# Performance work log

Hardware: AMD Instinct MI355X
Metric: run time of the kernel (lower is better)

Reference implementation:

```python
import jax, jax.numpy as jnp
import numpy as np

ENC_DIM, DEC_DIM, ATT_DIM = 2048, 512, 512
B, L = 64, 1024


def setup_inputs() -> dict:
    key = jax.random.key(0)
    ks = jax.random.split(key, 8)
    s_enc = 1.0 / np.sqrt(ENC_DIM)
    s_dec = 1.0 / np.sqrt(DEC_DIM)
    s_att = 1.0 / np.sqrt(ATT_DIM)
    return {
        "encoder_out": jax.random.normal(ks[0], (B, L, ENC_DIM), jnp.float32),
        "decoder_hidden": jax.random.normal(ks[1], (B, DEC_DIM), jnp.float32),
        "W_enc": jax.random.uniform(ks[2], (ENC_DIM, ATT_DIM), jnp.float32, -s_enc, s_enc),
        "b_enc": jax.random.uniform(ks[3], (ATT_DIM,), jnp.float32, -s_enc, s_enc),
        "W_dec": jax.random.uniform(ks[4], (DEC_DIM, ATT_DIM), jnp.float32, -s_dec, s_dec),
        "b_dec": jax.random.uniform(ks[5], (ATT_DIM,), jnp.float32, -s_dec, s_dec),
        "W_full": jax.random.uniform(ks[6], (ATT_DIM,), jnp.float32, -s_att, s_att),
        "b_full": jax.random.uniform(ks[7], (), jnp.float32, -s_att, s_att),
    }


def reference(encoder_out, decoder_hidden, W_enc, b_enc, W_dec, b_dec, W_full, b_full):
    # att1: [B, L, A]
    att1 = jnp.einsum('ble,ea->bla', encoder_out, W_enc) + b_enc
    # att2: [B, A]
    att2 = decoder_hidden @ W_dec + b_dec
    # scores: [B, L]
    att = jnp.einsum('bla,a->bl', jnp.tanh(att1 + att2[:, None, :]), W_full) + b_full
    alpha = jax.nn.softmax(att, axis=1)
    # NOTE: faithful to source -- weighted sum is over att1, not encoder_out.
    attention_weighted_encoding = jnp.einsum('bla,bl->ba', att1, alpha)
    return attention_weighted_encoding, alpha
```

## Files before the change

kernel.cpp:

```cpp
#include <hip/hip_runtime.h>
#include <hip/hip_bf16.h>


#define Bn 64
#define Ln 1024
#define En 2048
#define An 512
#define TM 64
#define NTILES (Ln/TM)
#define AWE_OFF 0
#define ALPHA_OFF (Bn*An)
#define TILEB 8192

using short8 = __attribute__((ext_vector_type(8))) short;
using f32x4  = __attribute__((ext_vector_type(4))) float;

__device__ inline short f2bf(float x){
    unsigned u = __builtin_bit_cast(unsigned, x);
    unsigned r = (u + 0x7fffu + ((u >> 16) & 1u)) >> 16;
    return (short)r;
}
__device__ inline float tanh_fast(float x){
    return 2.0f * __frcp_rn(1.0f + __expf(-2.0f * x)) - 1.0f;
}

__global__ __launch_bounds__(256) void k_prep(const float* __restrict__ W,
                                              unsigned short* __restrict__ Wp,
                                              const float* __restrict__ dh,
                                              const float* __restrict__ Wd,
                                              const float* __restrict__ bd,
                                              float* __restrict__ att2){
    __shared__ float dl[512];
    int blk = blockIdx.x, tid = threadIdx.x;
    if (blk < 512){
        int t = blk * 256 + tid;
        int f = t >> 6, lane = t & 63;
        int kb = f >> 5, nc = f & 31;
        int k0 = kb * 32 + (lane >> 4) * 8;
        int col = nc * 16 + (lane & 15);
        short8 v;
#pragma unroll
        for (int j = 0; j < 8; ++j)
            v[j] = f2bf(W[(size_t)(k0 + j) * An + col]);
        *(short8*)(Wp + (size_t)f * 512 + lane * 8) = v;
    } else {
        int b = blk - 512;
        dl[tid]       = dh[b * 512 + tid];
        dl[tid + 256] = dh[b * 512 + tid + 256];
        __syncthreads();
        for (int a = tid; a < An; a += 256){
            float s = bd[a];
            for (int k = 0; k < 512; ++k)
                s = fmaf(dl[k], Wd[(size_t)k * An + a], s);
            att2[b * An + a] = s;
        }
    }
}


#define MFMA(a, b, c) __builtin_amdgcn_mfma_f32_16x16x32_bf16((a), (b), (c), 0, 0, 0)

#define BLOAD(P)                                                              \
    { int pc = (P) > 31 ? 31 : (P);                                           \
      const unsigned short* bp = Bbase + (size_t)pc * 32768;                  \
      f00 = *(const short8*)(bp);                                             \
      f01 = *(const short8*)(bp + 512);                                       \
      f02 = *(const short8*)(bp + 1024);                                      \
      f03 = *(const short8*)(bp + 1536);                                      \
      f10 = *(const short8*)(bp + 16384);                                     \
      f11 = *(const short8*)(bp + 16384 + 512);                               \
      f12 = *(const short8*)(bp + 16384 + 1024);                              \
      f13 = *(const short8*)(bp + 16384 + 1536); }

#define STAGE(Q, R0, R1)                                                      \
    { short8 sv;                                                              \
      sv[0] = f2bf(R0.x); sv[1] = f2bf(R0.y);                                 \
      sv[2] = f2bf(R0.z); sv[3] = f2bf(R0.w);                                 \
      sv[4] = f2bf(R1.x); sv[5] = f2bf(R1.y);                                 \
      sv[6] = f2bf(R1.z); sv[7] = f2bf(R1.w);                                 \
      *(short8*)(swp + (Q) * TILEB) = sv; }

#define MFMAS(Q)                                                              \
    __builtin_amdgcn_s_setprio(1);                                            \
    _Pragma("unroll")                                                         \
    for (int mi = 0; mi < 4; ++mi){                                           \
        short8 af0 = *(const short8*)(as0 + (Q) * TILEB + mi * 2048);         \
        short8 af1 = *(const short8*)(as1 + (Q) * TILEB + mi * 2048);         \
        acc[mi][0] = MFMA(af0, f00, acc[mi][0]);                              \
        acc[mi][1] = MFMA(af0, f01, acc[mi][1]);                              \
        acc[mi][2] = MFMA(af0, f02, acc[mi][2]);                              \
        acc[mi][3] = MFMA(af0, f03, acc[mi][3]);                              \
        acc[mi][0] = MFMA(af1, f10, acc[mi][0]);                              \
        acc[mi][1] = MFMA(af1, f11, acc[mi][1]);                              \
        acc[mi][2] = MFMA(af1, f12, acc[mi][2]);                              \
        acc[mi][3] = MFMA(af1, f13, acc[mi][3]);                              \
    }                                                                         \
    __builtin_amdgcn_s_setprio(0);

#define PBAR                                                                  \
    __builtin_amdgcn_sched_barrier(0);                                        \
    asm volatile("s_waitcnt lgkmcnt(0)");                                     \
    __builtin_amdgcn_s_barrier();                                             \
    __builtin_amdgcn_sched_barrier(0)

__global__ __launch_bounds__(1024)
void k_main(const float* __restrict__ enc, const unsigned short* __restrict__ Wp,
            const float* __restrict__ benc, const float* __restrict__ att2,
            const float* __restrict__ wfull, float* __restrict__ out,
            float* __restrict__ pawe_ws, float* __restrict__ ms_ws){
    const int wg   = blockIdx.x;
    const int b    = wg >> 4;
    const int tile = wg & 15;
    const int l0   = tile * TM;
    const int tid  = threadIdx.x;
    const int lane = tid & 63, w = tid >> 6;
    const bool cons = (w < 8);

    __shared__ alignas(16) unsigned short Alds[4][TM * 64];
    __shared__ float red[8][TM];
    __shared__ float plds[TM];
    char* const alds = (char*)Alds;

    const int ptid  = tid & 511;
    const int srow  = ptid >> 3;
    const int sbyte = srow * 128 + (((ptid & 7) * 16) ^ ((srow & 7) << 4));
    char* const swp = alds + sbyte;
    const float* apt = enc + ((size_t)(b * Ln + l0 + srow)) * En + (ptid & 7) * 8;

    const unsigned short* Bbase = Wp + (size_t)((w & 7) * 4) * 512 + lane * 8;
    const int arow = lane & 15;
    const int akb  = (lane >> 4) * 16;
    const int sw   = (arow & 7) << 4;
    const char* const as0 = alds + arow * 128 + (akb ^ sw);
    const char* const as1 = alds + arow * 128 + ((64 + akb) ^ sw);

    f32x4 acc[4][4];
#pragma unroll
    for (int mi = 0; mi < 4; ++mi)
#pragma unroll
        for (int ni = 0; ni < 4; ++ni)
            acc[mi][ni] = (f32x4){0.f, 0.f, 0.f, 0.f};

    if (cons){
        short8 f00, f01, f02, f03, f10, f11, f12, f13;
        PBAR;
        for (int sp = 0; sp < 8; ++sp){
            const int p = sp * 4;
            BLOAD(p)        MFMAS(0)
            BLOAD(p + 1)    MFMAS(1)
            PBAR;
            BLOAD(p + 2)    MFMAS(2)
            BLOAD(p + 3)    MFMAS(3)
            PBAR;
        }
    } else {
        float4 ra0 = *(const float4*)(apt);
        float4 ra1 = *(const float4*)(apt + 4);
        float4 rb0 = *(const float4*)(apt + 64);
        float4 rb1 = *(const float4*)(apt + 68);
        STAGE(0, ra0, ra1)
        STAGE(1, rb0, rb1)
        ra0 = *(const float4*)(apt + 2 * 64);
        ra1 = *(const float4*)(apt + 2 * 64 + 4);
        rb0 = *(const float4*)(apt + 3 * 64);
        rb1 = *(const float4*)(apt + 3 * 64 + 4);
        PBAR;
        for (int sp = 0; sp < 8; ++sp){
            const int p = sp * 4;
            {
                STAGE(2, ra0, ra1)
                STAGE(3, rb0, rb1)
                int t0 = p + 4 > 31 ? 31 : p + 4;
                int t1 = p + 5 > 31 ? 31 : p + 5;
                ra0 = *(const float4*)(apt + t0 * 64);
                ra1 = *(const float4*)(apt + t0 * 64 + 4);
                rb0 = *(const float4*)(apt + t1 * 64);
                rb1 = *(const float4*)(apt + t1 * 64 + 4);
            }
            PBAR;
            {
                STAGE(0, ra0, ra1)
                STAGE(1, rb0, rb1)
                int t0 = p + 6 > 31 ? 31 : p + 6;
                int t1 = p + 7 > 31 ? 31 : p + 7;
                ra0 = *(const float4*)(apt + t0 * 64);
                ra1 = *(const float4*)(apt + t0 * 64 + 4);
                rb0 = *(const float4*)(apt + t1 * 64);
                rb1 = *(const float4*)(apt + t1 * 64 + 4);
            }
            PBAR;
        }
    }

    float tsum[4][4];
    if (cons){
        float be[4], a2[4], wfv[4];
        const int cbase = (w & 7) * 64 + (lane & 15);
#pragma unroll
        for (int ni = 0; ni < 4; ++ni){
            int c = cbase + ni * 16;
            be[ni]  = benc[c];
            a2[ni]  = att2[b * An + c];
            wfv[ni] = wfull[c];
        }
#pragma unroll
        for (int mi = 0; mi < 4; ++mi)
#pragma unroll
            for (int j = 0; j < 4; ++j)
                tsum[mi][j] = 0.f;
#pragma unroll
        for (int mi = 0; mi < 4; ++mi)
#pragma unroll
            for (int ni = 0; ni < 4; ++ni)
#pragma unroll
                for (int j = 0; j < 4; ++j){
                    float vv = acc[mi][ni][j] + be[ni];
                    acc[mi][ni][j] = vv;
                    tsum[mi][j] += tanh_fast(vv + a2[ni]) * wfv[ni];
                }
#pragma unroll
        for (int mi = 0; mi < 4; ++mi)
#pragma unroll
            for (int j = 0; j < 4; ++j){
                float t = tsum[mi][j];
                t += __shfl_xor(t, 1); t += __shfl_xor(t, 2);
                t += __shfl_xor(t, 4); t += __shfl_xor(t, 8);
                if ((lane & 15) == 0)
                    red[w][mi * 16 + (lane >> 4) * 4 + j] = t;
            }
    }
    __syncthreads();

    if (tid < 64){
        float s = 0.f;
#pragma unroll
        for (int k = 0; k < 8; ++k)
            s += red[k][tid];
        out[ALPHA_OFF + b * Ln + l0 + tid] = s;
        float m = s;
        m = fmaxf(m, __shfl_xor(m, 1));  m = fmaxf(m, __shfl_xor(m, 2));
        m = fmaxf(m, __shfl_xor(m, 4));  m = fmaxf(m, __shfl_xor(m, 8));
        m = fmaxf(m, __shfl_xor(m, 16)); m = fmaxf(m, __shfl_xor(m, 32));
        float pv = __expf(s - m);
        float sm = pv;
        sm += __shfl_xor(sm, 1);  sm += __shfl_xor(sm, 2);
        sm += __shfl_xor(sm, 4);  sm += __shfl_xor(sm, 8);
        sm += __shfl_xor(sm, 16); sm += __shfl_xor(sm, 32);
        plds[tid] = pv;
        if (tid == 0){ ms_ws[wg * 2] = m; ms_ws[wg * 2 + 1] = sm; }
    }
    __syncthreads();

    if (cons){
        float pp[4];
#pragma unroll
        for (int ni = 0; ni < 4; ++ni) pp[ni] = 0.f;
#pragma unroll
        for (int mi = 0; mi < 4; ++mi)
#pragma unroll
            for (int j = 0; j < 4; ++j){
                float pr = plds[mi * 16 + (lane >> 4) * 4 + j];
#pragma unroll
                for (int ni = 0; ni < 4; ++ni)
                    pp[ni] += pr * acc[mi][ni][j];
            }
#pragma unroll
        for (int ni = 0; ni < 4; ++ni){
            pp[ni] += __shfl_xor(pp[ni], 16);
            pp[ni] += __shfl_xor(pp[ni], 32);
        }
        if (lane < 16){
#pragma unroll
            for (int ni = 0; ni < 4; ++ni)
                pawe_ws[(size_t)wg * An + (w & 7) * 64 + ni * 16 + lane] = pp[ni];
        }
    }
}

__global__ __launch_bounds__(256) void k_final(const float* __restrict__ pawe,
                                               const float* __restrict__ ms,
                                               float* __restrict__ out){
    int b = blockIdx.x, tid = threadIdx.x;
    __shared__ float scale[NTILES];
    __shared__ float sh[2];
    if (tid < 64){
        int lane = tid;
        float m = -1e30f, su = 0.f;
        if (lane < NTILES){ m = ms[(b * NTILES + lane) * 2]; su = ms[(b * NTILES + lane) * 2 + 1]; }
        float mm = m;
        mm = fmaxf(mm, __shfl_xor(mm, 1)); mm = fmaxf(mm, __shfl_xor(mm, 2));
        mm = fmaxf(mm, __shfl_xor(mm, 4)); mm = fmaxf(mm, __shfl_xor(mm, 8));
        float sc = (lane < NTILES) ? su * __expf(m - mm) : 0.f;
        float tot = sc;
        tot += __shfl_xor(tot, 1); tot += __shfl_xor(tot, 2);
        tot += __shfl_xor(tot, 4); tot += __shfl_xor(tot, 8);
        if (lane < NTILES) scale[lane] = __expf(m - mm);
        if (lane == 0){ sh[0] = 1.0f / tot; sh[1] = mm; }
    }
    __syncthreads();
    float inv = sh[0], mm = sh[1];
    for (int a = tid; a < An; a += 256){
        float s = 0.f;
#pragma unroll
        for (int t = 0; t < NTILES; ++t)
            s += pawe[((size_t)(b * NTILES + t)) * An + a] * scale[t];
        out[AWE_OFF + b * An + a] = s * inv;
    }
    for (int l = tid; l < Ln; l += 256){
        float s = out[ALPHA_OFF + b * Ln + l];
        out[ALPHA_OFF + b * Ln + l] = __expf(s - mm) * inv;
    }
}

extern "C" void kernel_launch(void* const* d_in, const int* in_sizes, int n_in,
                              void* d_out, int out_size, void* d_ws, size_t ws_size,
                              hipStream_t stream){
    const float* enc   = (const float*)d_in[0];
    const float* dh    = (const float*)d_in[1];
    const float* Wenc  = (const float*)d_in[2];
    const float* benc  = (const float*)d_in[3];
    const float* Wdec  = (const float*)d_in[4];
    const float* bdec  = (const float*)d_in[5];
    const float* wfull = (const float*)d_in[6];
    float* out = (float*)d_out;

    char* ws = (char*)d_ws;
    unsigned short* Wp = (unsigned short*)ws;
    float* att2 = (float*)(ws + (2u << 20));
    float* pawe = (float*)(ws + (2u << 20) + (128u << 10));
    float* msb  = (float*)(ws + (4u << 20) + (128u << 10));

    k_prep<<<576, 256, 0, stream>>>(Wenc, Wp, dh, Wdec, bdec, att2);
    k_main<<<Bn * NTILES, 1024, 0, stream>>>(enc, Wp, benc, att2, wfull, out, pawe, msb);
    k_final<<<Bn, 256, 0, stream>>>(pawe, msb, out);
}
```

Baseline: 258.2 us.

## Merge producer and consumer waves so each wave stages A and runs MFMAs

The main kernel no longer splits its 16 waves into 8 loader waves (global fp32 load, bf16 convert, LDS store) and 8 MFMA waves. It now launches 512 threads per block, and every wave both stages the encoder tile into LDS and issues the weight loads and MFMAs, interleaved inside one loop. Launch bounds change to (512, 4) to allow several blocks per CU. This is meant to remove idle loader waves and rely on multiple resident blocks for latency hiding, at the cost of higher per-wave register pressure and less explicit producer/consumer overlap.

```diff
diff --git a/kernel.cpp b/kernel.cpp
--- a/kernel.cpp
+++ b/kernel.cpp
@@ -60,7 +60,7 @@
 
 #define MFMA(a, b, c) __builtin_amdgcn_mfma_f32_16x16x32_bf16((a), (b), (c), 0, 0, 0)
 
-#define BLOAD(P)                                                              \
+#define BLOADF(P)                                                             \
     { int pc = (P) > 31 ? 31 : (P);                                           \
       const unsigned short* bp = Bbase + (size_t)pc * 32768;                  \
       f00 = *(const short8*)(bp);                                             \
@@ -103,7 +103,7 @@
     __builtin_amdgcn_s_barrier();                                             \
     __builtin_amdgcn_sched_barrier(0)
 
-__global__ __launch_bounds__(1024)
+__global__ __launch_bounds__(512, 4)
 void k_main(const float* __restrict__ enc, const unsigned short* __restrict__ Wp,
             const float* __restrict__ benc, const float* __restrict__ att2,
             const float* __restrict__ wfull, float* __restrict__ out,
@@ -114,121 +114,119 @@
     const int l0   = tile * TM;
     const int tid  = threadIdx.x;
     const int lane = tid & 63, w = tid >> 6;
-    const bool cons = (w < 8);
 
     __shared__ alignas(16) unsigned short Alds[4][TM * 64];
     __shared__ float red[8][TM];
     __shared__ float plds[TM];
     char* const alds = (char*)Alds;
 
-    const int ptid  = tid & 511;
-    const int srow  = ptid >> 3;
-    const int sbyte = srow * 128 + (((ptid & 7) * 16) ^ ((srow & 7) << 4));
+    f32x4 acc[4][4];
+#pragma unroll
+    for (int mi = 0; mi < 4; ++mi)
+#pragma unroll
+        for (int ni = 0; ni < 4; ++ni)
+            acc[mi][ni] = (f32x4){0.f, 0.f, 0.f, 0.f};
+
+    const int srow  = tid >> 3;
+    const int sbyte = srow * 128 + (((tid & 7) * 16) ^ ((srow & 7) << 4));
     char* const swp = alds + sbyte;
-    const float* apt = enc + ((size_t)(b * Ln + l0 + srow)) * En + (ptid & 7) * 8;
-
-    const unsigned short* Bbase = Wp + (size_t)((w & 7) * 4) * 512 + lane * 8;
+    const float* apt = enc + ((size_t)(b * Ln + l0 + srow)) * En + (tid & 7) * 8;
+
+    const unsigned short* Bbase = Wp + (size_t)(w * 4) * 512 + lane * 8;
+
     const int arow = lane & 15;
     const int akb  = (lane >> 4) * 16;
     const int sw   = (arow & 7) << 4;
     const char* const as0 = alds + arow * 128 + (akb ^ sw);
     const char* const as1 = alds + arow * 128 + ((64 + akb) ^ sw);
 
-    f32x4 acc[4][4];
+    short8 f00, f01, f02, f03, f10, f11, f12, f13;
+
+    float4 ra0 = *(const float4*)(apt);
+    float4 ra1 = *(const float4*)(apt + 4);
+    float4 rb0 = *(const float4*)(apt + 64);
+    float4 rb1 = *(const float4*)(apt + 68);
+    STAGE(0, ra0, ra1)
+    STAGE(1, rb0, rb1)
+    ra0 = *(const float4*)(apt + 2 * 64);
+    ra1 = *(const float4*)(apt + 2 * 64 + 4);
+    rb0 = *(const float4*)(apt + 3 * 64);
+    rb1 = *(const float4*)(apt + 3 * 64 + 4);
+
+    for (int p = 0; p < 32; p += 4){
+        PBAR;
+        {
+            BLOADF(p)
+            STAGE(2, ra0, ra1)
+            STAGE(3, rb0, rb1)
+            int t0 = p + 4 > 31 ? 31 : p + 4;
+            int t1 = p + 5 > 31 ? 31 : p + 5;
+            ra0 = *(const float4*)(apt + t0 * 64);
+            ra1 = *(const float4*)(apt + t0 * 64 + 4);
+            rb0 = *(const float4*)(apt + t1 * 64);
+            rb1 = *(const float4*)(apt + t1 * 64 + 4);
+            MFMAS(0)
+        }
+        {
+            BLOADF(p + 1)
+            MFMAS(1)
+        }
+        PBAR;
+        {
+            BLOADF(p + 2)
+            STAGE(0, ra0, ra1)
+            STAGE(1, rb0, rb1)
+            int t0 = p + 6 > 31 ? 31 : p + 6;
+            int t1 = p + 7 > 31 ? 31 : p + 7;
+            ra0 = *(const float4*)(apt + t0 * 64);
+            ra1 = *(const float4*)(apt + t0 * 64 + 4);
+            rb0 = *(const float4*)(apt + t1 * 64);
+            rb1 = *(const float4*)(apt + t1 * 64 + 4);
+            MFMAS(2)
+        }
+        {
+            BLOADF(p + 3)
+            MFMAS(3)
+        }
+    }
+
+    float be[4], a2[4], wfv[4];
+    const int cbase = w * 64 + (lane & 15);
+#pragma unroll
+    for (int ni = 0; ni < 4; ++ni){
+        int c = cbase + ni * 16;
+        be[ni]  = benc[c];
+        a2[ni]  = att2[b * An + c];
+        wfv[ni] = wfull[c];
+    }
+
+    float tsum[4][4];
+#pragma unroll
+    for (int mi = 0; mi < 4; ++mi)
+#pragma unroll
+        for (int j = 0; j < 4; ++j)
+            tsum[mi][j] = 0.f;
 #pragma unroll
     for (int mi = 0; mi < 4; ++mi)
 #pragma unroll
         for (int ni = 0; ni < 4; ++ni)
-            acc[mi][ni] = (f32x4){0.f, 0.f, 0.f, 0.f};
-
-    if (cons){
-        short8 f00, f01, f02, f03, f10, f11, f12, f13;
-        PBAR;
-        for (int sp = 0; sp < 8; ++sp){
-            const int p = sp * 4;
-            BLOAD(p)        MFMAS(0)
-            BLOAD(p + 1)    MFMAS(1)
-            PBAR;
-            BLOAD(p + 2)    MFMAS(2)
-            BLOAD(p + 3)    MFMAS(3)
-            PBAR;
-        }
-    } else {
-        float4 ra0 = *(const float4*)(apt);
-        float4 ra1 = *(const float4*)(apt + 4);
-        float4 rb0 = *(const float4*)(apt + 64);
-        float4 rb1 = *(const float4*)(apt + 68);
-        STAGE(0, ra0, ra1)
-        STAGE(1, rb0, rb1)
-        ra0 = *(const float4*)(apt + 2 * 64);
-        ra1 = *(const float4*)(apt + 2 * 64 + 4);
-        rb0 = *(const float4*)(apt + 3 * 64);
-        rb1 = *(const float4*)(apt + 3 * 64 + 4);
-        PBAR;
-        for (int sp = 0; sp < 8; ++sp){
-            const int p = sp * 4;
-            {
-                STAGE(2, ra0, ra1)
-                STAGE(3, rb0, rb1)
-                int t0 = p + 4 > 31 ? 31 : p + 4;
-                int t1 = p + 5 > 31 ? 31 : p + 5;
-                ra0 = *(const float4*)(apt + t0 * 64);
-                ra1 = *(const float4*)(apt + t0 * 64 + 4);
-                rb0 = *(const float4*)(apt + t1 * 64);
-                rb1 = *(const float4*)(apt + t1 * 64 + 4);
+#pragma unroll
+            for (int j = 0; j < 4; ++j){
+                float vv = acc[mi][ni][j] + be[ni];
+                acc[mi][ni][j] = vv;
+                tsum[mi][j] += tanh_fast(vv + a2[ni]) * wfv[ni];
             }
-            PBAR;
-            {
-                STAGE(0, ra0, ra1)
-                STAGE(1, rb0, rb1)
-                int t0 = p + 6 > 31 ? 31 : p + 6;
-                int t1 = p + 7 > 31 ? 31 : p + 7;
-                ra0 = *(const float4*)(apt + t0 * 64);
-                ra1 = *(const float4*)(apt + t0 * 64 + 4);
-                rb0 = *(const float4*)(apt + t1 * 64);
-                rb1 = *(const float4*)(apt + t1 * 64 + 4);
-            }
-            PBAR;
-        }
-    }
-
-    float tsum[4][4];
-    if (cons){
-        float be[4], a2[4], wfv[4];
-        const int cbase = (w & 7) * 64 + (lane & 15);
-#pragma unroll
-        for (int ni = 0; ni < 4; ++ni){
-            int c = cbase + ni * 16;
-            be[ni]  = benc[c];
-            a2[ni]  = att2[b * An + c];
-            wfv[ni] = wfull[c];
-        }
-#pragma unroll
-        for (int mi = 0; mi < 4; ++mi)
-#pragma unroll
-            for (int j = 0; j < 4; ++j)
-                tsum[mi][j] = 0.f;
-#pragma unroll
-        for (int mi = 0; mi < 4; ++mi)
-#pragma unroll
-            for (int ni = 0; ni < 4; ++ni)
-#pragma unroll
-                for (int j = 0; j < 4; ++j){
-                    float vv = acc[mi][ni][j] + be[ni];
-                    acc[mi][ni][j] = vv;
-                    tsum[mi][j] += tanh_fast(vv + a2[ni]) * wfv[ni];
-                }
-#pragma unroll
-        for (int mi = 0; mi < 4; ++mi)
-#pragma unroll
-            for (int j = 0; j < 4; ++j){
-                float t = tsum[mi][j];
-                t += __shfl_xor(t, 1); t += __shfl_xor(t, 2);
-                t += __shfl_xor(t, 4); t += __shfl_xor(t, 8);
-                if ((lane & 15) == 0)
-                    red[w][mi * 16 + (lane >> 4) * 4 + j] = t;
-            }
-    }
+
+#pragma unroll
+    for (int mi = 0; mi < 4; ++mi)
+#pragma unroll
+        for (int j = 0; j < 4; ++j){
+            float t = tsum[mi][j];
+            t += __shfl_xor(t, 1); t += __shfl_xor(t, 2);
+            t += __shfl_xor(t, 4); t += __shfl_xor(t, 8);
+            if ((lane & 15) == 0)
+                red[w][mi * 16 + (lane >> 4) * 4 + j] = t;
+        }
     __syncthreads();
 
     if (tid < 64){
@@ -251,29 +249,27 @@
     }
     __syncthreads();
 
-    if (cons){
-        float pp[4];
-#pragma unroll
-        for (int ni = 0; ni < 4; ++ni) pp[ni] = 0.f;
-#pragma unroll
-        for (int mi = 0; mi < 4; ++mi)
-#pragma unroll
-            for (int j = 0; j < 4; ++j){
-                float pr = plds[mi * 16 + (lane >> 4) * 4 + j];
-#pragma unroll
-                for (int ni = 0; ni < 4; ++ni)
-                    pp[ni] += pr * acc[mi][ni][j];
-            }
-#pragma unroll
-        for (int ni = 0; ni < 4; ++ni){
-            pp[ni] += __shfl_xor(pp[ni], 16);
-            pp[ni] += __shfl_xor(pp[ni], 32);
-        }
-        if (lane < 16){
+    float pp[4];
+#pragma unroll
+    for (int ni = 0; ni < 4; ++ni) pp[ni] = 0.f;
+#pragma unroll
+    for (int mi = 0; mi < 4; ++mi)
+#pragma unroll
+        for (int j = 0; j < 4; ++j){
+            float pr = plds[mi * 16 + (lane >> 4) * 4 + j];
 #pragma unroll
             for (int ni = 0; ni < 4; ++ni)
-                pawe_ws[(size_t)wg * An + (w & 7) * 64 + ni * 16 + lane] = pp[ni];
-        }
+                pp[ni] += pr * acc[mi][ni][j];
+        }
+#pragma unroll
+    for (int ni = 0; ni < 4; ++ni){
+        pp[ni] += __shfl_xor(pp[ni], 16);
+        pp[ni] += __shfl_xor(pp[ni], 32);
+    }
+    if (lane < 16){
+#pragma unroll
+        for (int ni = 0; ni < 4; ++ni)
+            pawe_ws[(size_t)wg * An + w * 64 + ni * 16 + lane] = pp[ni];
     }
 }
 
@@ -331,6 +327,6 @@
     float* msb  = (float*)(ws + (4u << 20) + (128u << 10));
 
     k_prep<<<576, 256, 0, stream>>>(Wenc, Wp, dh, Wdec, bdec, att2);
-    k_main<<<Bn * NTILES, 1024, 0, stream>>>(enc, Wp, benc, att2, wfull, out, pawe, msb);
+    k_main<<<Bn * NTILES, 512, 0, stream>>>(enc, Wp, benc, att2, wfull, out, pawe, msb);
     k_final<<<Bn, 256, 0, stream>>>(pawe, msb, out);
 }
```

After: 377.7 us. 1.46x slower.
